# Performance work log

Hardware: AMD Instinct MI355X
Metric: run time of the kernel (lower is better)

## Reference

```python
import jax, jax.numpy as jnp
import numpy as np

B, N, V = 8, 2000, 2000
K = 100            # local_size
EMB = 128          # ff_hidden_dim
PENALTY = -1e9
EPS = 1e-5         # InstanceNorm eps


def setup_inputs() -> dict:
    key = jax.random.key(0)
    ks = jax.random.split(key, 16)
    s = 0.02
    return {
        "dist": jax.random.uniform(ks[0], (B, N, V), dtype=jnp.float32),
        "theta": jax.random.normal(ks[1], (B, N, V), dtype=jnp.float32),
        "scale": jax.random.uniform(ks[2], (B, N, 1), dtype=jnp.float32),
        # Linear params stored [in, out]
        "w1": jax.random.normal(ks[3], (2 * K + 1, EMB), dtype=jnp.float32) * s,
        "b1": jnp.zeros((EMB,), jnp.float32),
        "w2": jax.random.normal(ks[4], (EMB, 2 * EMB), dtype=jnp.float32) * s,
        "b2": jnp.zeros((2 * EMB,), jnp.float32),
        "w3": jax.random.normal(ks[5], (2 * EMB, EMB), dtype=jnp.float32) * s,
        "b3": jnp.zeros((EMB,), jnp.float32),
        "w4": jax.random.normal(ks[6], (EMB, K), dtype=jnp.float32) * s,
        "b4": jnp.zeros((K,), jnp.float32),
        "gamma": jnp.ones((2 * EMB,), jnp.float32),   # InstanceNorm affine weight
        "beta": jnp.zeros((2 * EMB,), jnp.float32),   # InstanceNorm affine bias
    }


def reference(dist, theta, scale, w1, b1, w2, b2, w3, b3, w4, b4, gamma, beta):
    # --- topk smallest distances (ascending) + gather theta ---
    neg_vals, idx = jax.lax.top_k(-dist, K)          # [B,N,K]
    sorted_dist = -neg_vals                           # ascending k smallest
    sorted_dist = sorted_dist / jnp.max(sorted_dist, axis=-1, keepdims=True)
    sorted_theta = jnp.take_along_axis(theta, idx, axis=-1)  # [B,N,K]

    # --- small MLP with InstanceNorm over the node dim ---
    x_in = jnp.concatenate([sorted_dist, sorted_theta, scale], axis=-1)  # [B,N,2K+1]
    emb = jax.nn.relu(x_in @ w1 + b1)                 # [B,N,EMB]
    h = jax.nn.relu(emb @ w2 + b2)                    # [B,N,2*EMB]
    # InstanceNorm1d: normalize each channel over the length (node) dim, biased var
    mean = jnp.mean(h, axis=1, keepdims=True)
    var = jnp.var(h, axis=1, keepdims=True)
    h = (h - mean) * jax.lax.rsqrt(var + EPS) * gamma + beta
    emb = jax.nn.relu(h @ w3 + b3)                    # [B,N,EMB]
    out = (emb @ w4 + b4) - sorted_dist               # [B,N,K]

    # --- scatter into penalty-initialized matrix ---
    out_mat = jnp.full((B, N, V), PENALTY, dtype=dist.dtype)
    b_ix = jnp.arange(B)[:, None, None]
    n_ix = jnp.arange(N)[None, :, None]
    return out_mat.at[b_ix, n_ix, idx].set(out)
```

## Files before the change

kernel.cpp:

```cpp
#include <hip/hip_runtime.h>
#include <hip/hip_bf16.h>

#define BB 8
#define NN 2000
#define VV 2000
#define KK 100
#define EMB 128
#define PENALTY -1e9f
#define NBIN 512
#define BINSCALE 2048.0f
#define CAP 200
#define XPAD 224

typedef __attribute__((ext_vector_type(8))) short short8;
typedef __attribute__((ext_vector_type(4))) float f32x4;

#define WB() __builtin_amdgcn_wave_barrier()

__device__ __forceinline__ unsigned short bf16rne(float f) {
    unsigned u = __float_as_uint(f);
    u += 0x7FFF + ((u >> 16) & 1);
    return (unsigned short)(u >> 16);
}
__device__ __forceinline__ float bf2f(unsigned short s) {
    return __uint_as_float((unsigned)s << 16);
}

#define FORALL_VALS(BODY)                                                    \
    _Pragma("unroll") for (int c = 0; c < 8; ++c) {                          \
        { const float fv = v4[c].x; const int e = (c * 64 + lane) * 4 + 0; BODY } \
        { const float fv = v4[c].y; const int e = (c * 64 + lane) * 4 + 1; BODY } \
        { const float fv = v4[c].z; const int e = (c * 64 + lane) * 4 + 2; BODY } \
        { const float fv = v4[c].w; const int e = (c * 64 + lane) * 4 + 3; BODY } \
    }

__global__ __launch_bounds__(256) void wpack_kernel(
    const float* __restrict__ w1, const float* __restrict__ w2,
    const float* __restrict__ w3, const float* __restrict__ w4,
    unsigned short* __restrict__ pw1, unsigned short* __restrict__ pw2,
    unsigned short* __restrict__ pw3, unsigned short* __restrict__ pw4)
{
    const int bt = blockIdx.x;
    const int t = threadIdx.x;
    for (int e = t; e < 512; e += 256) {
        int lane = e >> 3, j = e & 7;
        int kk = ((lane >> 4) << 3) + j;
        int nn = lane & 15;
        if (bt < 56) {
            int kt = bt >> 3, nt = bt & 7;
            int k = kt * 32 + kk, n = nt * 16 + nn;
            float f = (k < 201) ? w1[k * 128 + n] : 0.f;
            pw1[bt * 512 + e] = bf16rne(f);
        } else if (bt < 120) {
            int bb = bt - 56, kt = bb >> 4, nt = bb & 15;
            pw2[bb * 512 + e] = bf16rne(w2[(kt * 32 + kk) * 256 + nt * 16 + nn]);
        } else if (bt < 184) {
            int bb = bt - 120, kt = bb >> 3, nt = bb & 7;
            pw3[bb * 512 + e] = bf16rne(w3[(kt * 32 + kk) * 128 + nt * 16 + nn]);
        } else {
            int bb = bt - 184, kt = bb / 7, nt = bb % 7;
            int n = nt * 16 + nn;
            float f = (n < 100) ? w4[(kt * 32 + kk) * 100 + n] : 0.f;
            pw4[bb * 512 + e] = bf16rne(f);
        }
    }
}

__global__ __launch_bounds__(256) void topk_kernel(
    const float* __restrict__ dist, const float* __restrict__ theta,
    const float* __restrict__ scale,
    unsigned short* __restrict__ xin, float* __restrict__ sdist,
    int* __restrict__ idxb)
{
    __shared__ __align__(16) unsigned hist[4][NBIN];
    __shared__ __align__(16) unsigned binstart[4][NBIN];
    __shared__ unsigned long long comp[4][CAP];
    __shared__ unsigned long long comp2[4][CAP];
    __shared__ int sh_cnt[4], sh_ntie[4], sh_kth[4];
    __shared__ unsigned sh_pref[4];
    __shared__ int sh_tie[4][64];

    const int t = threadIdx.x;
    const int w = t >> 6, lane = t & 63;
    const int row = blockIdx.x * 4 + w;
    const float4* d4 = (const float4*)(dist + (size_t)row * VV);

    float4 v4[8];
#pragma unroll
    for (int c = 0; c < 7; ++c) v4[c] = d4[c * 64 + lane];
    v4[7] = (lane < 52) ? d4[448 + lane] : make_float4(2.f, 2.f, 2.f, 2.f);

    {
        uint4 z = make_uint4(0u, 0u, 0u, 0u);
        *(uint4*)&hist[w][lane * 8] = z;
        *(uint4*)&hist[w][lane * 8 + 4] = z;
    }
    if (lane == 0) { sh_cnt[w] = 0; sh_ntie[w] = 0; }
    WB();

    FORALL_VALS({
        int b = (int)(fv * BINSCALE);
        b = b < 0 ? 0 : b;
        if (b < NBIN - 1) atomicAdd(&hist[w][b], 1u);
        (void)e;
    });
    WB();

    uint4 h0 = *(const uint4*)&hist[w][lane * 8];
    uint4 h1 = *(const uint4*)&hist[w][lane * 8 + 4];
    unsigned c8[8] = {h0.x, h0.y, h0.z, h0.w, h1.x, h1.y, h1.z, h1.w};
    unsigned tot = 0;
#pragma unroll
    for (int b = 0; b < 8; ++b) tot += c8[b];
    unsigned incl = tot;
#pragma unroll
    for (int off = 1; off < 64; off <<= 1) {
        unsigned v = __shfl_up(incl, (unsigned)off);
        if (lane >= off) incl += v;
    }
    const unsigned excl = incl - tot;

    int myBt = -1, myM = 0;
    {
        unsigned runv = excl;
        unsigned st[8];
#pragma unroll
        for (int b = 0; b < 8; ++b) {
            st[b] = runv;
            if (myBt < 0 && runv < KK && runv + c8[b] >= KK) {
                myBt = lane * 8 + b;
                myM = (int)(runv + c8[b]);
            }
            runv += c8[b];
        }
        uint4 s0 = make_uint4(st[0], st[1], st[2], st[3]);
        uint4 s1 = make_uint4(st[4], st[5], st[6], st[7]);
        *(uint4*)&hist[w][lane * 8] = s0;
        *(uint4*)&hist[w][lane * 8 + 4] = s1;
        *(uint4*)&binstart[w][lane * 8] = s0;
        *(uint4*)&binstart[w][lane * 8 + 4] = s1;
    }
    WB();

    unsigned long long bl = __ballot(myBt >= 0);
    int Bt, m;
    if (bl != 0ull) {
        int src = __ffsll(bl) - 1;
        Bt = __shfl(myBt, src);
        m = __shfl(myM, src);
    } else {
        Bt = NBIN - 1;
        m = 100000;
    }

    if (m <= CAP) {
        FORALL_VALS({
            int b = (int)(fv * BINSCALE);
            b = b < 0 ? 0 : (b > NBIN - 1 ? NBIN - 1 : b);
            if (b <= Bt) {
                int slot = (int)atomicAdd(&hist[w][b], 1u);
                comp[w][slot] =
                    ((unsigned long long)__float_as_uint(fv) << 32) | (unsigned)e;
            }
        });
        WB();
        FORALL_VALS({
            int b = (int)(fv * BINSCALE);
            b = b < 0 ? 0 : (b > NBIN - 1 ? NBIN - 1 : b);
            if (b <= Bt) {
                unsigned long long key =
                    ((unsigned long long)__float_as_uint(fv) << 32) | (unsigned)e;
                unsigned s0 = binstart[w][b];
                unsigned e0 = hist[w][b];
                int r = (int)s0;
                for (unsigned s = s0; s < e0; ++s) r += (comp[w][s] < key);
                comp2[w][r] = key;
            }
        });
    } else {
        FORALL_VALS({
            int b = (int)(fv * BINSCALE);
            b = b < 0 ? 0 : (b > NBIN - 1 ? NBIN - 1 : b);
            if (b < Bt) {
                int pos = atomicAdd(&sh_cnt[w], 1);
                if (pos < CAP)
                    comp[w][pos] =
                        ((unsigned long long)__float_as_uint(fv) << 32) | (unsigned)e;
            }
        });
        WB();
        int nless = sh_cnt[w];
        if (lane == 0) { sh_pref[w] = 0u; sh_kth[w] = KK - nless; }
        WB();
        for (int p = 0; p < 4; ++p) {
            { uint4 z = make_uint4(0u, 0u, 0u, 0u); *(uint4*)&hist[w][lane * 4] = z; }
            WB();
            const int shift = 24 - 8 * p;
            const unsigned pref = sh_pref[w];
            FORALL_VALS({
                int b = (int)(fv * BINSCALE);
                b = b < 0 ? 0 : (b > NBIN - 1 ? NBIN - 1 : b);
                if (b == Bt) {
                    unsigned k = __float_as_uint(fv);
                    bool ok = (p == 0) || ((k >> (shift + 8)) == pref);
                    if (ok) atomicAdd(&hist[w][(k >> shift) & 255u], 1u);
                }
                (void)e;
            });
            WB();
            if (lane == 0) {
                int kth = sh_kth[w];
                unsigned cum = 0;
                int b = 0;
                for (; b < 256; ++b) {
                    unsigned cc = hist[w][b];
                    if (cum + cc >= (unsigned)kth) break;
                    cum += cc;
                }
                sh_pref[w] = (pref << 8) | (unsigned)b;
                sh_kth[w] = kth - (int)cum;
            }
            WB();
        }
        const unsigned T = sh_pref[w];
        const int need2 = sh_kth[w];
        FORALL_VALS({
            int b = (int)(fv * BINSCALE);
            b = b < 0 ? 0 : (b > NBIN - 1 ? NBIN - 1 : b);
            if (b == Bt) {
                unsigned k = __float_as_uint(fv);
                if (k < T) {
                    int pos = atomicAdd(&sh_cnt[w], 1);
                    if (pos < CAP)
                        comp[w][pos] = ((unsigned long long)k << 32) | (unsigned)e;
                } else if (k == T) {
                    int q = atomicAdd(&sh_ntie[w], 1);
                    if (q < 64) sh_tie[w][q] = e;
                }
            }
        });
        WB();
        if (lane == 0) {
            int nl2 = sh_cnt[w];
            int nt = sh_ntie[w] < 64 ? sh_ntie[w] : 64;
            for (int i = 1; i < nt; ++i) {
                int v = sh_tie[w][i], j2 = i - 1;
                while (j2 >= 0 && sh_tie[w][j2] > v) {
                    sh_tie[w][j2 + 1] = sh_tie[w][j2];
                    --j2;
                }
                sh_tie[w][j2 + 1] = v;
            }
            for (int i = 0; i < need2; ++i)
                comp[w][nl2 + i] =
                    ((unsigned long long)T << 32) | (unsigned)sh_tie[w][i];
            sh_cnt[w] = nl2 + need2;
        }
        WB();
        const int mm = sh_cnt[w];
        for (int o = lane; o < mm; o += 64) {
            unsigned long long key = comp[w][o];
            int r = 0;
            for (int j2 = 0; j2 < mm; ++j2) {
                unsigned long long cj = comp[w][j2];
                r += (cj < key) || (cj == key && j2 < o);
            }
            if (r < CAP) comp2[w][r] = key;
        }
    }
    WB();

    const float Tf = __uint_as_float((unsigned)(comp2[w][KK - 1] >> 32));
    const float invT = 1.0f / Tf;
    const float* trow = theta + (size_t)row * VV;
    for (int o = lane; o < KK; o += 64) {
        unsigned long long c = comp2[w][o];
        unsigned kbits = (unsigned)(c >> 32);
        int id = (int)(c & 0xFFFFFFFFu);
        float nv = __uint_as_float(kbits) * invT;
        xin[(size_t)row * XPAD + o] = bf16rne(nv);
        xin[(size_t)row * XPAD + 100 + o] = bf16rne(trow[id]);
        sdist[(size_t)row * KK + o] = nv;
        idxb[(size_t)row * KK + o] = id;
    }
    if (lane == 0) xin[(size_t)row * XPAD + 200] = bf16rne(scale[row]);
    else if (lane < 24) xin[(size_t)row * XPAD + 200 + lane] = 0;
}

__global__ __launch_bounds__(256) void fused12_mfma(
    const unsigned short* __restrict__ xin, const unsigned short* __restrict__ pw1,
    const float* __restrict__ b1, const unsigned short* __restrict__ pw2,
    const float* __restrict__ b2, unsigned short* __restrict__ h)
{
    __shared__ unsigned short c1s[64][136];
    const int t = threadIdx.x;
    const int w = t >> 6, l = t & 63;
    const int m0 = blockIdx.x * 64;
    const int lr = l & 15, lg = l >> 4;

    f32x4 acc[8] = {};
    const short8* arow = (const short8*)(xin + (size_t)(m0 + 16 * w + lr) * XPAD);
    const short8* pw1v = (const short8*)pw1;
#pragma unroll
    for (int kt = 0; kt < 7; ++kt) {
        short8 a = arow[kt * 4 + lg];
#pragma unroll
        for (int nt = 0; nt < 8; ++nt) {
            short8 b = pw1v[(kt * 8 + nt) * 64 + l];
            acc[nt] = __builtin_amdgcn_mfma_f32_16x16x32_bf16(a, b, acc[nt], 0, 0, 0);
        }
    }
#pragma unroll
    for (int nt = 0; nt < 8; ++nt) {
        int col = nt * 16 + lr;
        float bb = b1[col];
#pragma unroll
        for (int r = 0; r < 4; ++r) {
            float v = fmaxf(acc[nt][r] + bb, 0.f);
            c1s[16 * w + lg * 4 + r][col] = bf16rne(v);
        }
    }
    __syncthreads();

    f32x4 acc2[16] = {};
    const short8* pw2v = (const short8*)pw2;
#pragma unroll
    for (int kt = 0; kt < 4; ++kt) {
        short8 a = *(const short8*)&c1s[16 * w + lr][kt * 32 + lg * 8];
#pragma unroll
        for (int nt = 0; nt < 16; ++nt) {
            short8 b = pw2v[(kt * 16 + nt) * 64 + l];
            acc2[nt] = __builtin_amdgcn_mfma_f32_16x16x32_bf16(a, b, acc2[nt], 0, 0, 0);
        }
    }
#pragma unroll
    for (int nt = 0; nt < 16; ++nt) {
        int col = nt * 16 + lr;
        float bb = b2[col];
#pragma unroll
        for (int r = 0; r < 4; ++r) {
            float v = fmaxf(acc2[nt][r] + bb, 0.f);
            h[(size_t)(m0 + 16 * w + lg * 4 + r) * 256 + col] = bf16rne(v);
        }
    }
}

#define NCHUNK 25
#define CHUNK (NN / NCHUNK)

__global__ __launch_bounds__(256) void stats_partial(
    const unsigned short* __restrict__ h, float* __restrict__ part)
{
    const int b = blockIdx.x, ch = blockIdx.y, c = threadIdx.x;
    const unsigned short* base = h + ((size_t)b * NN + (size_t)ch * CHUNK) * 256 + c;
    float s = 0.f, s2 = 0.f;
    for (int n = 0; n < CHUNK; ++n) {
        float v = bf2f(base[(size_t)n * 256]);
        s += v;
        s2 += v * v;
    }
    size_t o = (((size_t)b * NCHUNK + ch) * 256 + c) * 2;
    part[o] = s;
    part[o + 1] = s2;
}

__global__ __launch_bounds__(256) void stats_final(
    const float* __restrict__ part, const float* __restrict__ gamma,
    const float* __restrict__ beta, float* __restrict__ scv,
    float* __restrict__ shv)
{
    const int b = blockIdx.x, c = threadIdx.x;
    float s = 0.f, s2 = 0.f;
    for (int ch = 0; ch < NCHUNK; ++ch) {
        size_t o = (((size_t)b * NCHUNK + ch) * 256 + c) * 2;
        s += part[o];
        s2 += part[o + 1];
    }
    const float inv = 1.0f / (float)NN;
    float mean = s * inv;
    float var = s2 * inv - mean * mean;
    float rs = rsqrtf(var + 1e-5f);
    float sc = gamma[c] * rs;
    scv[b * 256 + c] = sc;
    shv[b * 256 + c] = beta[c] - mean * sc;
}

__global__ __launch_bounds__(256) void fused34_mfma(
    const unsigned short* __restrict__ h, const unsigned short* __restrict__ pw3,
    const float* __restrict__ b3, const unsigned short* __restrict__ pw4,
    const float* __restrict__ b4, const float* __restrict__ scv,
    const float* __restrict__ shv, const float* __restrict__ sdist,
    const int* __restrict__ idxb, float* __restrict__ out)
{
    __shared__ __align__(16) char uni[64 * 100 * 4];
    __shared__ __align__(16) unsigned bm[64][64];
    __shared__ __align__(16) unsigned short wpref[64][64];
    unsigned short (*c1s)[136] = (unsigned short (*)[136])uni;
    float (*valbuf)[100] = (float (*)[100])uni;

    const int t = threadIdx.x;
    const int w = t >> 6, l = t & 63;
    const int m0 = blockIdx.x * 64;
    const int lr = l & 15, lg = l >> 4;

    for (int i = t; i < 64 * 64; i += 256) ((unsigned*)bm)[i] = 0u;
    __syncthreads();

    for (int i = t; i < 64 * KK; i += 256) {
        int rrow = i / KK;
        int id = idxb[(size_t)(m0 + rrow) * KK + (i - rrow * KK)];
        atomicOr(&bm[rrow][id >> 5], 1u << (id & 31));
    }

    const int myrow = m0 + 16 * w + lr;
    const int mybatch = myrow / NN;

    f32x4 acc[8] = {};
    const short8* hrow = (const short8*)(h + (size_t)myrow * 256);
    const short8* pw3v = (const short8*)pw3;
#pragma unroll
    for (int kt = 0; kt < 8; ++kt) {
        int k0 = kt * 32 + lg * 8;
        short8 hv = hrow[kt * 4 + lg];
        const float4* scp = (const float4*)(scv + mybatch * 256 + k0);
        const float4* shp = (const float4*)(shv + mybatch * 256 + k0);
        float4 sc0 = scp[0], sc1 = scp[1];
        float4 sh0 = shp[0], sh1 = shp[1];
        short8 a;
        a[0] = (short)bf16rne(fmaf(bf2f((unsigned short)hv[0]), sc0.x, sh0.x));
        a[1] = (short)bf16rne(fmaf(bf2f((unsigned short)hv[1]), sc0.y, sh0.y));
        a[2] = (short)bf16rne(fmaf(bf2f((unsigned short)hv[2]), sc0.z, sh0.z));
        a[3] = (short)bf16rne(fmaf(bf2f((unsigned short)hv[3]), sc0.w, sh0.w));
        a[4] = (short)bf16rne(fmaf(bf2f((unsigned short)hv[4]), sc1.x, sh1.x));
        a[5] = (short)bf16rne(fmaf(bf2f((unsigned short)hv[5]), sc1.y, sh1.y));
        a[6] = (short)bf16rne(fmaf(bf2f((unsigned short)hv[6]), sc1.z, sh1.z));
        a[7] = (short)bf16rne(fmaf(bf2f((unsigned short)hv[7]), sc1.w, sh1.w));
#pragma unroll
        for (int nt = 0; nt < 8; ++nt) {
            short8 b = pw3v[(kt * 8 + nt) * 64 + l];
            acc[nt] = __builtin_amdgcn_mfma_f32_16x16x32_bf16(a, b, acc[nt], 0, 0, 0);
        }
    }
    __syncthreads();

    if (t < 64) {
        unsigned run = 0;
#pragma unroll
        for (int wd = 0; wd < 63; ++wd) {
            wpref[t][wd] = (unsigned short)run;
            run += (unsigned)__popc(bm[t][wd]);
        }
        wpref[t][63] = (unsigned short)run;
    }

#pragma unroll
    for (int nt = 0; nt < 8; ++nt) {
        int col = nt * 16 + lr;
        float bb = b3[col];
#pragma unroll
        for (int r = 0; r < 4; ++r) {
            float v = fmaxf(acc[nt][r] + bb, 0.f);
            c1s[16 * w + lg * 4 + r][col] = bf16rne(v);
        }
    }
    __syncthreads();

    f32x4 acc2[7] = {};
    const short8* pw4v = (const short8*)pw4;
#pragma unroll
    for (int kt = 0; kt < 4; ++kt) {
        short8 a = *(const short8*)&c1s[16 * w + lr][kt * 32 + lg * 8];
#pragma unroll
        for (int nt = 0; nt < 7; ++nt) {
            short8 b = pw4v[(kt * 7 + nt) * 64 + l];
            acc2[nt] = __builtin_amdgcn_mfma_f32_16x16x32_bf16(a, b, acc2[nt], 0, 0, 0);
        }
    }
    __syncthreads();

#pragma unroll
    for (int nt = 0; nt < 7; ++nt) {
        int col = nt * 16 + lr;
        if (col < KK) {
            float bb = b4[col];
#pragma unroll
            for (int r = 0; r < 4; ++r) {
                int r4 = 16 * w + lg * 4 + r;
                int mrow = m0 + r4;
                float v = acc2[nt][r] + bb - sdist[(size_t)mrow * KK + col];
                int id = idxb[(size_t)mrow * KK + col];
                int wd = id >> 5;
                int irank = (int)wpref[r4][wd] +
                            __popc(bm[r4][wd] & ((1u << (id & 31)) - 1u));
                valbuf[r4][irank] = v;
            }
        }
    }
    __syncthreads();

    for (int i = t; i < 64 * (VV / 4); i += 256) {
        int rrow = i / (VV / 4);
        int p = i - rrow * (VV / 4);
        int v0 = p * 4;
        unsigned word = bm[rrow][v0 >> 5];
        int sh = v0 & 31;
        int racc = (int)wpref[rrow][v0 >> 5] + __popc(word & ((1u << sh) - 1u));
        float4 o;
        unsigned b0 = (word >> sh) & 1u;
        o.x = b0 ? valbuf[rrow][racc] : PENALTY; racc += b0;
        unsigned b1_ = (word >> (sh + 1)) & 1u;
        o.y = b1_ ? valbuf[rrow][racc] : PENALTY; racc += b1_;
        unsigned b2_ = (word >> (sh + 2)) & 1u;
        o.z = b2_ ? valbuf[rrow][racc] : PENALTY; racc += b2_;
        unsigned b3_ = (word >> (sh + 3)) & 1u;
        o.w = b3_ ? valbuf[rrow][racc] : PENALTY;
        ((float4*)(out + (size_t)(m0 + rrow) * VV))[p] = o;
    }
}

extern "C" void kernel_launch(void* const* d_in, const int* in_sizes, int n_in,
                              void* d_out, int out_size, void* d_ws, size_t ws_size,
                              hipStream_t stream)
{
    const float* dist  = (const float*)d_in[0];
    const float* theta = (const float*)d_in[1];
    const float* scale = (const float*)d_in[2];
    const float* w1 = (const float*)d_in[3];
    const float* b1 = (const float*)d_in[4];
    const float* w2 = (const float*)d_in[5];
    const float* b2 = (const float*)d_in[6];
    const float* w3 = (const float*)d_in[7];
    const float* b3 = (const float*)d_in[8];
    const float* w4 = (const float*)d_in[9];
    const float* b4 = (const float*)d_in[10];
    const float* gamma = (const float*)d_in[11];
    const float* beta  = (const float*)d_in[12];
    float* out = (float*)d_out;

    const int M = BB * NN;

    char* p = (char*)d_ws;
    unsigned short* xin = (unsigned short*)p;       p += (size_t)M * XPAD * 2;
    unsigned short* h   = (unsigned short*)p;       p += (size_t)M * 256 * 2;
    float* sdist = (float*)p;                       p += (size_t)M * KK * 4;
    int*   idxb  = (int*)p;                         p += (size_t)M * KK * 4;
    float* part  = (float*)p;                       p += (size_t)BB * NCHUNK * 256 * 2 * 4;
    float* scv   = (float*)p;                       p += 8 * 256 * 4;
    float* shv   = (float*)p;                       p += 8 * 256 * 4;
    unsigned short* pw1 = (unsigned short*)p;       p += 56 * 512 * 2;
    unsigned short* pw2 = (unsigned short*)p;       p += 64 * 512 * 2;
    unsigned short* pw3 = (unsigned short*)p;       p += 64 * 512 * 2;
    unsigned short* pw4 = (unsigned short*)p;       p += 28 * 512 * 2;

    wpack_kernel<<<212, 256, 0, stream>>>(w1, w2, w3, w4, pw1, pw2, pw3, pw4);

    topk_kernel<<<M / 4, 256, 0, stream>>>(dist, theta, scale, xin, sdist, idxb);

    fused12_mfma<<<M / 64, 256, 0, stream>>>(xin, pw1, b1, pw2, b2, h);

    stats_partial<<<dim3(BB, NCHUNK), 256, 0, stream>>>(h, part);
    stats_final<<<BB, 256, 0, stream>>>(part, gamma, beta, scv, shv);

    fused34_mfma<<<M / 64, 256, 0, stream>>>(h, pw3, b3, pw4, b4, scv, shv,
                                             sdist, idxb, out);
}
```

Measured before the change: 151.4 us.

## Shrink top-k LDS footprint and split theta gather into separate kernel

The top-k kernel drops the per-bin start array and stores 8-bit bin counts instead, deriving each bin's start from its end minus its count. The second compaction buffer shrinks to K entries, with writes beyond rank K discarded. Together these cut shared memory per block to allow more resident blocks. The random theta gather moves out of the top-k kernel into its own fully parallel kernel over all B*N*K elements, at the cost of an extra launch and a reread of the index buffer.

```diff
diff --git a/kernel.cpp b/kernel.cpp
--- a/kernel.cpp
+++ b/kernel.cpp
@@ -67,15 +67,14 @@
 }
 
 __global__ __launch_bounds__(256) void topk_kernel(
-    const float* __restrict__ dist, const float* __restrict__ theta,
-    const float* __restrict__ scale,
+    const float* __restrict__ dist, const float* __restrict__ scale,
     unsigned short* __restrict__ xin, float* __restrict__ sdist,
     int* __restrict__ idxb)
 {
     __shared__ __align__(16) unsigned hist[4][NBIN];
-    __shared__ __align__(16) unsigned binstart[4][NBIN];
+    __shared__ __align__(8) unsigned char cnt8[4][NBIN];
     __shared__ unsigned long long comp[4][CAP];
-    __shared__ unsigned long long comp2[4][CAP];
+    __shared__ unsigned long long comp2[4][KK + 4];
     __shared__ int sh_cnt[4], sh_ntie[4], sh_kth[4];
     __shared__ unsigned sh_pref[4];
     __shared__ int sh_tie[4][64];
@@ -133,12 +132,13 @@
             }
             runv += c8[b];
         }
-        uint4 s0 = make_uint4(st[0], st[1], st[2], st[3]);
-        uint4 s1 = make_uint4(st[4], st[5], st[6], st[7]);
-        *(uint4*)&hist[w][lane * 8] = s0;
-        *(uint4*)&hist[w][lane * 8 + 4] = s1;
-        *(uint4*)&binstart[w][lane * 8] = s0;
-        *(uint4*)&binstart[w][lane * 8 + 4] = s1;
+        *(uint4*)&hist[w][lane * 8] = make_uint4(st[0], st[1], st[2], st[3]);
+        *(uint4*)&hist[w][lane * 8 + 4] = make_uint4(st[4], st[5], st[6], st[7]);
+        unsigned p0 = (c8[0] & 255u) | ((c8[1] & 255u) << 8) |
+                      ((c8[2] & 255u) << 16) | ((c8[3] & 255u) << 24);
+        unsigned p1 = (c8[4] & 255u) | ((c8[5] & 255u) << 8) |
+                      ((c8[6] & 255u) << 16) | ((c8[7] & 255u) << 24);
+        *(uint2*)&cnt8[w][lane * 8] = make_uint2(p0, p1);
     }
     WB();
 
@@ -170,11 +170,11 @@
             if (b <= Bt) {
                 unsigned long long key =
                     ((unsigned long long)__float_as_uint(fv) << 32) | (unsigned)e;
-                unsigned s0 = binstart[w][b];
                 unsigned e0 = hist[w][b];
+                unsigned s0 = e0 - (unsigned)cnt8[w][b];
                 int r = (int)s0;
                 for (unsigned s = s0; s < e0; ++s) r += (comp[w][s] < key);
-                comp2[w][r] = key;
+                if (r < KK) comp2[w][r] = key;
             }
         });
     } else {
@@ -265,26 +265,36 @@
                 unsigned long long cj = comp[w][j2];
                 r += (cj < key) || (cj == key && j2 < o);
             }
-            if (r < CAP) comp2[w][r] = key;
+            if (r < KK) comp2[w][r] = key;
         }
     }
     WB();
 
     const float Tf = __uint_as_float((unsigned)(comp2[w][KK - 1] >> 32));
     const float invT = 1.0f / Tf;
-    const float* trow = theta + (size_t)row * VV;
     for (int o = lane; o < KK; o += 64) {
         unsigned long long c = comp2[w][o];
         unsigned kbits = (unsigned)(c >> 32);
         int id = (int)(c & 0xFFFFFFFFu);
         float nv = __uint_as_float(kbits) * invT;
         xin[(size_t)row * XPAD + o] = bf16rne(nv);
-        xin[(size_t)row * XPAD + 100 + o] = bf16rne(trow[id]);
         sdist[(size_t)row * KK + o] = nv;
         idxb[(size_t)row * KK + o] = id;
     }
     if (lane == 0) xin[(size_t)row * XPAD + 200] = bf16rne(scale[row]);
     else if (lane < 24) xin[(size_t)row * XPAD + 200 + lane] = 0;
+}
+
+__global__ __launch_bounds__(256) void gather_kernel(
+    const float* __restrict__ theta, const int* __restrict__ idxb,
+    unsigned short* __restrict__ xin)
+{
+    const int i = blockIdx.x * 256 + threadIdx.x;
+    const int row = i / KK;
+    const int k = i - row * KK;
+    const int id = idxb[i];
+    float v = theta[(size_t)row * VV + id];
+    xin[(size_t)row * XPAD + 100 + k] = bf16rne(v);
 }
 
 __global__ __launch_bounds__(256) void fused12_mfma(
@@ -554,7 +564,9 @@
 
     wpack_kernel<<<212, 256, 0, stream>>>(w1, w2, w3, w4, pw1, pw2, pw3, pw4);
 
-    topk_kernel<<<M / 4, 256, 0, stream>>>(dist, theta, scale, xin, sdist, idxb);
+    topk_kernel<<<M / 4, 256, 0, stream>>>(dist, scale, xin, sdist, idxb);
+
+    gather_kernel<<<(M * KK) / 256, 256, 0, stream>>>(theta, idxb, xin);
 
     fused12_mfma<<<M / 64, 256, 0, stream>>>(xin, pw1, b1, pw2, b2, h);
 
```

After: 195.2 us. 1.29x slower.
